# Kernel tuning notes

Hardware: AMD Instinct MI355X
Metric: run time of the kernel (lower is better)

Reference implementation:

```python
import jax, jax.numpy as jnp
import numpy as np
import math

D_MODEL = 1024
NUM_HEADS = 16
HEAD_DIM = D_MODEL // NUM_HEADS
BATCH = 2
SEQ = 2048
THETA = 10000.0


def _rope_tables(seq_len, head_dim, theta=THETA):
    inv_freq = 1.0 / theta ** (jnp.arange(0, head_dim, 2, dtype=jnp.float32) / head_dim)
    pos = jnp.arange(seq_len, dtype=jnp.float32)
    freqs = jnp.outer(pos, inv_freq)                 # [S, hd/2]
    emb = jnp.concatenate([freqs, freqs], axis=-1)   # [S, hd]
    return jnp.cos(emb), jnp.sin(emb)


def _rotate_half(x):
    x1, x2 = jnp.split(x, 2, axis=-1)
    return jnp.concatenate([-x2, x1], axis=-1)


def setup_inputs() -> dict:
    key = jax.random.key(0)
    k1, k2, k3 = jax.random.split(key, 3)
    x = jax.random.normal(k1, (BATCH, SEQ, D_MODEL), dtype=jnp.float32)
    # causal mask: 1 where attend allowed, 0 where masked
    mask = jnp.tril(jnp.ones((SEQ, SEQ), dtype=jnp.int32))[None, None]
    w_qkv = jax.random.normal(k2, (D_MODEL, 3 * D_MODEL), dtype=jnp.float32) / math.sqrt(D_MODEL)
    w_out = jax.random.normal(k3, (D_MODEL, D_MODEL), dtype=jnp.float32) / math.sqrt(D_MODEL)
    return {"x": x, "mask": mask, "w_qkv": w_qkv, "w_out": w_out}


def reference(x, mask, w_qkv, w_out):
    B, S, _ = x.shape
    qkv = x @ w_qkv                                          # [B,S,3*D]
    qkv = qkv.reshape(B, S, 3, NUM_HEADS, HEAD_DIM)
    qkv = jnp.transpose(qkv, (2, 0, 3, 1, 4))                # [3,B,H,S,hd]
    q, k, v = qkv[0], qkv[1], qkv[2]
    cos, sin = _rope_tables(S, HEAD_DIM)                     # [S,hd]
    cos = cos[None, None]; sin = sin[None, None]
    q = q * cos + _rotate_half(q) * sin
    k = k * cos + _rotate_half(k) * sin
    scores = jnp.einsum('bhqd,bhkd->bhqk', q, k) / math.sqrt(HEAD_DIM)
    scores = jnp.where(mask == 0, -jnp.inf, scores)
    attn = jax.nn.softmax(scores, axis=-1)                   # dropout p=0 (eval)
    out = jnp.einsum('bhqk,bhkd->bhqd', attn, v)             # [B,H,S,hd]
    out = jnp.transpose(out, (0, 2, 1, 3)).reshape(B, S, D_MODEL)
    return out @ w_out
```

## Files before the change

### kernel.cpp

```cpp
#include <hip/hip_runtime.h>

typedef __bf16 bf16;
typedef __bf16 bf16x4 __attribute__((ext_vector_type(4)));
typedef __bf16 bf16x8 __attribute__((ext_vector_type(8)));
typedef short s16x4 __attribute__((ext_vector_type(4)));
typedef float f32x4 __attribute__((ext_vector_type(4)));

constexpr int BATCH = 2;
constexpr int SEQ   = 2048;
constexpr int DMODEL= 1024;
constexpr int NH    = 16;
constexpr int HD    = 64;
constexpr int M_ROWS= BATCH * SEQ;
constexpr int N_QKV = 3 * DMODEL;

#if defined(__HIP_DEVICE_COMPILE__) && __has_builtin(__builtin_amdgcn_exp2f)
#define EXP2(x) __builtin_amdgcn_exp2f(x)
#else
#define EXP2(x) exp2f(x)
#endif

__device__ __forceinline__ void gl_lds16(const bf16* g, bf16* l) {
  __builtin_amdgcn_global_load_lds(
      (const __attribute__((address_space(1))) unsigned int*)g,
      (__attribute__((address_space(3))) unsigned int*)l, 16, 0, 0);
}

__device__ __forceinline__ f32x4 mfma_16x16x16_bf16(bf16x4 a, bf16x4 b,
                                                    f32x4 c) {
#if defined(__HIP_DEVICE_COMPILE__)
  union { bf16x4 h; s16x4 s; } ua{a}, ub{b};
  return __builtin_amdgcn_mfma_f32_16x16x16bf16_1k(ua.s, ub.s, c, 0, 0, 0);
#else
  return c;
#endif
}

__global__ __launch_bounds__(256) void prep_kernel(
    const float* __restrict__ x, const float* __restrict__ w_qkv,
    const float* __restrict__ w_out, bf16* __restrict__ xb,
    bf16* __restrict__ WqkvT, bf16* __restrict__ WoutT) {
  const int bx = blockIdx.x, t = threadIdx.x;
  if (bx < 2048) {
    const int i = (bx * 256 + t) * 8;
    float4 f0 = *(const float4*)&x[i];
    float4 f1 = *(const float4*)&x[i + 4];
    bf16x8 v;
    v[0] = (bf16)f0.x; v[1] = (bf16)f0.y; v[2] = (bf16)f0.z; v[3] = (bf16)f0.w;
    v[4] = (bf16)f1.x; v[5] = (bf16)f1.y; v[6] = (bf16)f1.z; v[7] = (bf16)f1.w;
    *(bf16x8*)&xb[i] = v;
    return;
  }
  __shared__ float tile[32][33];
  const float* src;
  bf16* dst;
  int R, C, c0, r0;
  if (bx < 5120) {
    const int idx = bx - 2048;
    src = w_qkv; dst = WqkvT; R = DMODEL; C = N_QKV;
    c0 = (idx % 96) * 32; r0 = (idx / 96) * 32;
  } else {
    const int idx = bx - 5120;
    src = w_out; dst = WoutT; R = DMODEL; C = DMODEL;
    c0 = (idx & 31) * 32; r0 = (idx >> 5) * 32;
  }
  const int r = t >> 3, c4 = (t & 7) * 4;
  {
    float4 f = *(const float4*)&src[(size_t)(r0 + r) * C + c0 + c4];
    tile[r][c4 + 0] = f.x; tile[r][c4 + 1] = f.y;
    tile[r][c4 + 2] = f.z; tile[r][c4 + 3] = f.w;
  }
  __syncthreads();
  {
    bf16x4 v;
#pragma unroll
    for (int j = 0; j < 4; j++) v[j] = (bf16)tile[c4 + j][r];
    *(bf16x4*)&dst[(size_t)(c0 + r) * R + r0 + c4] = v;
  }
}

__global__ __launch_bounds__(256) void gemm_out64(
    const bf16* __restrict__ A, const bf16* __restrict__ BT,
    float* __restrict__ C, int M, int N, int K) {
  __shared__ bf16 As[2][2048];
  __shared__ bf16 Bs[2][4096];
  const int t = threadIdx.x;
  const int m0 = blockIdx.y * 64;
  const int n0 = blockIdx.x * 128;
  const int w = t >> 6, lane = t & 63, g = lane >> 4, li = lane & 15;
  const int r0w = (w & 1) * 32, c0w = (w >> 1) * 64;
  f32x4 acc[2][4] = {};
  const int ia = w * 64 + lane;
  const int ra = ia >> 2, ca = (ia & 3) * 8;
  const int ib0 = (w * 2 + 0) * 64 + lane, ib1 = (w * 2 + 1) * 64 + lane;
  const int rb0 = ib0 >> 2, cb0 = (ib0 & 3) * 8;
  const int rb1 = ib1 >> 2, cb1 = (ib1 & 3) * 8;

#define OUT_STAGE(buf, k0)                                                   \
  {                                                                          \
    gl_lds16(&A[(size_t)(m0 + ra) * K + (k0) + ca], &As[buf][w * 512]);      \
    gl_lds16(&BT[(size_t)(n0 + rb0) * K + (k0) + cb0],                       \
             &Bs[buf][(w * 2 + 0) * 512]);                                   \
    gl_lds16(&BT[(size_t)(n0 + rb1) * K + (k0) + cb1],                       \
             &Bs[buf][(w * 2 + 1) * 512]);                                   \
  }

  OUT_STAGE(0, 0);
  __syncthreads();
  for (int it = 0; it < 32; ++it) {
    const int cur = it & 1;
    if (it < 31) OUT_STAGE(cur ^ 1, (it + 1) * 32);
    bf16x8 a[2], b[4];
#pragma unroll
    for (int mt = 0; mt < 2; mt++)
      a[mt] = *(const bf16x8*)&As[cur][(r0w + mt * 16 + li) * 32 + g * 8];
#pragma unroll
    for (int nt = 0; nt < 4; nt++)
      b[nt] = *(const bf16x8*)&Bs[cur][(c0w + nt * 16 + li) * 32 + g * 8];
#pragma unroll
    for (int mt = 0; mt < 2; mt++)
#pragma unroll
      for (int nt = 0; nt < 4; nt++)
        acc[mt][nt] = __builtin_amdgcn_mfma_f32_16x16x32_bf16(
            a[mt], b[nt], acc[mt][nt], 0, 0, 0);
    __syncthreads();
  }
#undef OUT_STAGE

#pragma unroll
  for (int mt = 0; mt < 2; mt++)
#pragma unroll
    for (int nt = 0; nt < 4; nt++)
#pragma unroll
      for (int r = 0; r < 4; r++) {
        const int m = m0 + r0w + mt * 16 + g * 4 + r;
        const int n = n0 + c0w + nt * 16 + li;
        C[(size_t)m * N + n] = acc[mt][nt][r];
      }
}

__global__ __launch_bounds__(256) void gemm_qkv_rope(
    const bf16* __restrict__ A, const bf16* __restrict__ BT,
    bf16* __restrict__ Qb, bf16* __restrict__ Kb, bf16* __restrict__ Vt) {
  constexpr int K = DMODEL;
  __shared__ bf16 smem[16384];
  const int t = threadIdx.x;
  const int m0 = blockIdx.y * 128;
  const int n0 = blockIdx.x * 128;
  const int w = t >> 6, lane = t & 63, g = lane >> 4, li = lane & 15;
  const int r0w = (w & 1) * 64, c0w = (w >> 1) * 64;
  f32x4 acc[4][4] = {};

  const int i0 = (w * 2 + 0) * 64 + lane, i1 = (w * 2 + 1) * 64 + lane;
  const int sr0 = i0 >> 2, sc0 = (i0 & 3) * 8;
  const int sr1 = i1 >> 2, sc1 = (i1 & 3) * 8;

#define QKV_STAGE(buf, k0)                                                   \
  {                                                                          \
    bf16* Asb = smem + (buf)*4096;                                           \
    bf16* Bsb = smem + 8192 + (buf)*4096;                                    \
    gl_lds16(&A[(size_t)(m0 + sr0) * K + (k0) + sc0],                        \
             &Asb[(w * 2 + 0) * 512]);                                       \
    gl_lds16(&A[(size_t)(m0 + sr1) * K + (k0) + sc1],                        \
             &Asb[(w * 2 + 1) * 512]);                                       \
    gl_lds16(&BT[(size_t)(n0 + sr0) * K + (k0) + sc0],                       \
             &Bsb[(w * 2 + 0) * 512]);                                       \
    gl_lds16(&BT[(size_t)(n0 + sr1) * K + (k0) + sc1],                       \
             &Bsb[(w * 2 + 1) * 512]);                                       \
  }

  QKV_STAGE(0, 0);
  __syncthreads();
  for (int it = 0; it < 32; ++it) {
    const int cur = it & 1;
    if (it < 31) QKV_STAGE(cur ^ 1, (it + 1) * 32);
    const bf16* Asb = smem + cur * 4096;
    const bf16* Bsb = smem + 8192 + cur * 4096;
    bf16x8 a[4], b[4];
#pragma unroll
    for (int mt = 0; mt < 4; mt++)
      a[mt] = *(const bf16x8*)&Asb[(r0w + mt * 16 + li) * 32 + g * 8];
#pragma unroll
    for (int nt = 0; nt < 4; nt++)
      b[nt] = *(const bf16x8*)&Bsb[(c0w + nt * 16 + li) * 32 + g * 8];
#pragma unroll
    for (int mt = 0; mt < 4; mt++)
#pragma unroll
      for (int nt = 0; nt < 4; nt++)
        acc[mt][nt] = __builtin_amdgcn_mfma_f32_16x16x32_bf16(
            a[mt], b[nt], acc[mt][nt], 0, 0, 0);
    __syncthreads();
  }
#undef QKV_STAGE

  const int region = n0 >> 10;
  const int b = m0 >> 11;
  const int h = ((n0 + c0w) >> 6) & 15;
  const size_t bh = (size_t)(b * NH + h);

  if (region < 2) {
    bf16* dst = region == 0 ? Qb : Kb;
    const float outsc = region == 0 ? 0.125f * 1.44269504f : 1.f;
    const float L = 13.287712379549449f;
    const float if0 = exp2f(-(float)(2 * li) / 64.f * L);
    const float if1 = exp2f(-(float)(2 * (li + 16)) / 64.f * L);
    bf16* lw = smem + w * 2112;
#pragma unroll
    for (int pass = 0; pass < 2; pass++) {
      __syncthreads();
#pragma unroll
      for (int mtl = 0; mtl < 2; mtl++) {
        const int mt = pass * 2 + mtl;
#pragma unroll
        for (int r = 0; r < 4; r++) {
          const int s = (m0 + r0w + mt * 16 + g * 4 + r) & (SEQ - 1);
          float cs[2], sn[2];
          __sincosf((float)s * if0, &sn[0], &cs[0]);
          __sincosf((float)s * if1, &sn[1], &cs[1]);
#pragma unroll
          for (int nt = 0; nt < 4; nt++) {
            const int par = nt & 1;
            const float a = acc[mt][nt][r];
            const float ap = acc[mt][nt ^ 2][r];
            const float v = (nt < 2) ? a * cs[par] - ap * sn[par]
                                     : a * cs[par] + ap * sn[par];
            lw[(mtl * 16 + g * 4 + r) * 66 + nt * 16 + li] =
                (bf16)(v * outsc);
          }
        }
      }
      __syncthreads();
      const int rowl = lane >> 1, dh = (lane & 1) * 32;
      const int s = (m0 + r0w + pass * 32 + rowl) & (SEQ - 1);
      bf16* gdst = &dst[(bh * SEQ + s) * HD + dh];
      const bf16* lsrc = &lw[rowl * 66 + dh];
#pragma unroll
      for (int c = 0; c < 4; c++)
        *(bf16x8*)&gdst[c * 8] = *(const bf16x8*)&lsrc[c * 8];
    }
  } else {
#pragma unroll
    for (int mt = 0; mt < 4; mt++)
#pragma unroll
      for (int nt = 0; nt < 4; nt++) {
        const int s = (m0 + r0w + mt * 16 + g * 4) & (SEQ - 1);
        const int d = nt * 16 + li;
        bf16x4 v;
#pragma unroll
        for (int r = 0; r < 4; r++) v[r] = (bf16)acc[mt][nt][r];
        *(bf16x4*)&Vt[(bh * HD + d) * SEQ + s] = v;
      }
  }
}

__device__ const unsigned char CHUNK_TAB[80] = {
    124, 125, 126, 127,
    120, 121, 122, 116, 117, 118, 112, 113, 114, 108, 109, 110,
    104, 105, 106, 100, 101, 102, 96,  97,  98,  92,  93,  94,
    88,  89,  84,  85,  80,  81,  76,  77,  72,  73,  68,  69,
    64,  65,  60,  61,
    56,  52,  48,  44,  40,  36,  32,  28,
    24,  57,  90,  123, 20,  53,  86,  119, 16,  49,  82,  115,
    12,  45,  78,  111, 8,   41,  74,  107, 4,   37,  70,  103,
    0,   33,  66,  99};

__global__ __launch_bounds__(256, 5) void flash_attn15(
    const bf16* __restrict__ Q, const bf16* __restrict__ Kb,
    const bf16* __restrict__ Vt, bf16* __restrict__ Oout,
    float* __restrict__ Opart, float* __restrict__ Lpart) {
  const int bx = blockIdx.x;
  const unsigned char e = CHUNK_TAB[bx >> 5];
  const int qt = e >> 2, kch = e & 3;
  const int bh = bx & 31;
  const int q0 = qt * 64;
  const int jlo = kch * 8;
  const int jhi = min(jlo + 8, qt + 1);
  const int t = threadIdx.x, w = t >> 6, lane = t & 63, g = lane >> 4,
            li = lane & 15;

  __shared__ bf16 Ks[2][4096];
  __shared__ bf16 Vs[2][4096];

  const bf16* Qh = Q  + (size_t)bh * SEQ * HD;
  const bf16* Kh = Kb + (size_t)bh * SEQ * HD;
  const bf16* Vh = Vt + (size_t)bh * HD * SEQ;

  const int qw = q0 + w * 16;

  bf16x8 qf[2];
#pragma unroll
  for (int ks = 0; ks < 2; ks++)
    qf[ks] = *(const bf16x8*)&Qh[(size_t)(qw + li) * HD + ks * 32 + g * 8];

  f32x4 o[4] = {};
  f32x4 o4  = {};
  bf16x4 ones;
#pragma unroll
  for (int r = 0; r < 4; r++) ones[r] = (bf16)1.f;

  int koffB[2][4];
#pragma unroll
  for (int ks = 0; ks < 2; ks++)
#pragma unroll
    for (int nt = 0; nt < 4; nt++) {
      const int rK = nt * 16 + li;
      const int pK = rK * 8 + ((ks * 4 + g) ^ (li & 7));
      koffB[ks][nt] = pK * 16;
    }
  int voffB[4][4];
#pragma unroll
  for (int nt = 0; nt < 4; nt++)
#pragma unroll
    for (int dt = 0; dt < 4; dt++) {
      const int rV = dt * 16 + li;
      const int cg = nt * 2 + (g >> 1);
      const int pV = rV * 8 + (cg ^ (rV & 7));
      voffB[nt][dt] = pV * 16 + (g & 1) * 8;
    }

  const int p0 = w * 128 + lane, p1 = p0 + 64;
  const int sr0 = p0 >> 3, sc0 = ((p0 & 7) ^ (sr0 & 7)) * 8;
  const int sr1 = p1 >> 3, sc1 = ((p1 & 7) ^ (sr1 & 7)) * 8;
  const int lo0 = w * 1024, lo1 = w * 1024 + 512;

  {
    const int jn = jlo * 64;
    gl_lds16(&Kh[(size_t)(jn + sr0) * HD + sc0], &Ks[jlo & 1][lo0]);
    gl_lds16(&Kh[(size_t)(jn + sr1) * HD + sc1], &Ks[jlo & 1][lo1]);
    gl_lds16(&Vh[(size_t)sr0 * SEQ + jn + sc0], &Vs[jlo & 1][lo0]);
    gl_lds16(&Vh[(size_t)sr1 * SEQ + jn + sc1], &Vs[jlo & 1][lo1]);
  }
  __syncthreads();

  for (int ti = jlo; ti < jhi; ++ti) {
    const int cur = ti & 1, nxt = cur ^ 1;
    const char* ksb = (const char*)&Ks[cur][0];
    const char* vsb = (const char*)&Vs[cur][0];
    if (ti + 1 < jhi) {
      const int jn = ti * 64 + 64;
      gl_lds16(&Kh[(size_t)(jn + sr0) * HD + sc0], &Ks[nxt][lo0]);
      gl_lds16(&Kh[(size_t)(jn + sr1) * HD + sc1], &Ks[nxt][lo1]);
      gl_lds16(&Vh[(size_t)sr0 * SEQ + jn + sc0], &Vs[nxt][lo0]);
      gl_lds16(&Vh[(size_t)sr1 * SEQ + jn + sc1], &Vs[nxt][lo1]);
    }

    if (ti < qt) {
      f32x4 sacc[4] = {};
      __builtin_amdgcn_s_setprio(1);
#pragma unroll
      for (int ks = 0; ks < 2; ks++)
#pragma unroll
        for (int nt = 0; nt < 4; nt++) {
          bf16x8 kf = *(const bf16x8*)(ksb + koffB[ks][nt]);
          sacc[nt] = __builtin_amdgcn_mfma_f32_16x16x32_bf16(kf, qf[ks],
                                                             sacc[nt], 0, 0, 0);
        }
      __builtin_amdgcn_s_setprio(0);

      bf16x4 pf[4];
#pragma unroll
      for (int nt = 0; nt < 4; nt++)
#pragma unroll
        for (int r = 0; r < 4; r++) pf[nt][r] = (bf16)EXP2(sacc[nt][r]);

      __builtin_amdgcn_s_setprio(1);
#pragma unroll
      for (int nt = 0; nt < 4; nt++) {
        o4 = mfma_16x16x16_bf16(ones, pf[nt], o4);
#pragma unroll
        for (int dt = 0; dt < 4; dt++) {
          bf16x4 vfrag = *(const bf16x4*)(vsb + voffB[nt][dt]);
          o[dt] = mfma_16x16x16_bf16(vfrag, pf[nt], o[dt]);
        }
      }
      __builtin_amdgcn_s_setprio(0);
    } else {
      f32x4 sacc[4] = {};
      __builtin_amdgcn_s_setprio(1);
#pragma unroll
      for (int ks = 0; ks < 2; ks++)
#pragma unroll
        for (int nt = 0; nt < 4; nt++) {
          if (nt > w) continue;
          bf16x8 kf = *(const bf16x8*)(ksb + koffB[ks][nt]);
          sacc[nt] = __builtin_amdgcn_mfma_f32_16x16x32_bf16(kf, qf[ks],
                                                             sacc[nt], 0, 0, 0);
        }
      __builtin_amdgcn_s_setprio(0);

      bf16x4 pf[4];
#pragma unroll
      for (int nt = 0; nt < 4; nt++) {
        if (nt > w) continue;
#pragma unroll
        for (int r = 0; r < 4; r++) {
          float v = sacc[nt][r];
          if (nt == w) {
            const int kk = nt * 16 + g * 4 + r;
            v = (kk <= w * 16 + li) ? v : -1e30f;
          }
          pf[nt][r] = (bf16)EXP2(v);
        }
      }

      __builtin_amdgcn_s_setprio(1);
#pragma unroll
      for (int nt = 0; nt < 4; nt++) {
        if (nt > w) continue;
        o4 = mfma_16x16x16_bf16(ones, pf[nt], o4);
#pragma unroll
        for (int dt = 0; dt < 4; dt++) {
          bf16x4 vfrag = *(const bf16x4*)(vsb + voffB[nt][dt]);
          o[dt] = mfma_16x16x16_bf16(vfrag, pf[nt], o[dt]);
        }
      }
      __builtin_amdgcn_s_setprio(0);
    }
    __syncthreads();
  }

  if (qt <= 7) {
    const float inv_l = 1.f / o4[0];
    const int b = bh >> 4, h = bh & 15;
    const int s = qw + li;
#pragma unroll
    for (int dt = 0; dt < 4; dt++) {
      bf16x4 ov;
#pragma unroll
      for (int r = 0; r < 4; r++) ov[r] = (bf16)(o[dt][r] * inv_l);
      *(bf16x4*)&Oout[((size_t)(b * SEQ + s)) * DMODEL + h * 64 + dt * 16 +
                      g * 4] = ov;
    }
  } else {
    const int s = qw + li;
    int off;
    if (qt < 16)       off = (s - 512) * 2 + kch;
    else if (qt < 24)  off = 1024 + (s - 1024) * 3 + kch;
    else               off = 2560 + (s - 1536) * 4 + kch;
    const size_t slot = (size_t)bh * 4608 + off;
    if (g == 0) Lpart[slot] = o4[0];
    float* od = &Opart[slot * 64];
#pragma unroll
    for (int dt = 0; dt < 4; dt++)
      *(f32x4*)&od[dt * 16 + g * 4] = o[dt];
  }
}

__global__ __launch_bounds__(256) void attn_merge2(
    const float* __restrict__ Opart, const float* __restrict__ Lpart,
    bf16* __restrict__ attn) {
  const int gi = blockIdx.x * 256 + threadIdx.x;
  const int row = gi >> 3;
  const int d0 = (gi & 7) * 8;
  const int bh = row / 1536, srel = row - bh * 1536;
  const int b = bh >> 4, h = bh & 15, s = srel + 512;
  int off0, nc;
  if (srel < 512)       { off0 = srel * 2;                nc = 2; }
  else if (srel < 1024) { off0 = 1024 + (srel - 512) * 3; nc = 3; }
  else                  { off0 = 2560 + (srel - 1024) * 4; nc = 4; }
  const size_t base = (size_t)bh * 4608 + off0;
  float lsum = 0.f;
  float acc[8] = {};
  for (int c = 0; c < nc; c++) {
    lsum += Lpart[base + c];
    const float* p = &Opart[(base + c) * 64 + d0];
    float4 a0 = *(const float4*)p;
    float4 a1 = *(const float4*)(p + 4);
    acc[0] += a0.x; acc[1] += a0.y; acc[2] += a0.z; acc[3] += a0.w;
    acc[4] += a1.x; acc[5] += a1.y; acc[6] += a1.z; acc[7] += a1.w;
  }
  const float inv = 1.f / lsum;
  bf16x8 v;
#pragma unroll
  for (int i = 0; i < 8; i++) v[i] = (bf16)(acc[i] * inv);
  *(bf16x8*)&attn[((size_t)(b * SEQ + s)) * DMODEL + h * 64 + d0] = v;
}

extern "C" void kernel_launch(void* const* d_in, const int* in_sizes, int n_in,
                              void* d_out, int out_size, void* d_ws,
                              size_t ws_size, hipStream_t stream) {
  const float* x     = (const float*)d_in[0];
  const float* w_qkv = (const float*)d_in[2];
  const float* w_out = (const float*)d_in[3];
  float* out = (float*)d_out;

  char* ws = (char*)d_ws;
  bf16* WqkvT = (bf16*)(ws);
  bf16* WoutT = (bf16*)(ws + 6291456);
  bf16* xb    = (bf16*)(ws + 8388608);
  bf16* Qb    = (bf16*)(ws + 16777216);
  bf16* Kbuf  = (bf16*)(ws + 25165824);
  bf16* Vt    = (bf16*)(ws + 33554432);
  bf16* attn  = (bf16*)(ws + 41943040);
  float* Opart= (float*)(ws + 50331648);
  float* Lpart= (float*)(ws + 88080384);

  prep_kernel<<<dim3(6144), 256, 0, stream>>>(x, w_qkv, w_out, xb, WqkvT,
                                              WoutT);
  gemm_qkv_rope<<<dim3(N_QKV / 128, M_ROWS / 128), 256, 0, stream>>>(
      xb, WqkvT, Qb, Kbuf, Vt);
  flash_attn15<<<dim3(2560), 256, 0, stream>>>(Qb, Kbuf, Vt, attn, Opart,
                                               Lpart);
  attn_merge2<<<dim3(1536), 256, 0, stream>>>(Opart, Lpart, attn);
  gemm_out64<<<dim3(DMODEL / 128, M_ROWS / 64), 256, 0, stream>>>(
      attn, WoutT, out, M_ROWS, DMODEL, DMODEL);
}
```

Before: 194.2 us.

## Triple-buffer QKV GEMM with vmcnt waits; single-buffer output GEMM

The QKV+RoPE GEMM moves from a double-buffered to a three-stage LDS pipeline. It prefetches two K-slices ahead and replaces __syncthreads with explicit s_waitcnt vmcnt(4) plus s_barrier, so one slice of global-to-LDS loads can stay in flight across the barrier. This should hide more load latency, at the cost of 48KB of LDS per block, which may lower occupancy. Separately, the output-projection GEMM drops its double buffering and becomes a simple load, sync, compute loop, which removes its load/compute overlap.

Result: faster. 190.0 us (-2.2%).

```diff
diff --git a/kernel.cpp b/kernel.cpp
--- a/kernel.cpp
+++ b/kernel.cpp
@@ -82,51 +82,42 @@
 __global__ __launch_bounds__(256) void gemm_out64(
     const bf16* __restrict__ A, const bf16* __restrict__ BT,
     float* __restrict__ C, int M, int N, int K) {
-  __shared__ bf16 As[2][2048];
-  __shared__ bf16 Bs[2][4096];
+  __shared__ bf16 As[64 * 32];
+  __shared__ bf16 Bs[128 * 32];
   const int t = threadIdx.x;
   const int m0 = blockIdx.y * 64;
   const int n0 = blockIdx.x * 128;
   const int w = t >> 6, lane = t & 63, g = lane >> 4, li = lane & 15;
   const int r0w = (w & 1) * 32, c0w = (w >> 1) * 64;
   f32x4 acc[2][4] = {};
-  const int ia = w * 64 + lane;
-  const int ra = ia >> 2, ca = (ia & 3) * 8;
-  const int ib0 = (w * 2 + 0) * 64 + lane, ib1 = (w * 2 + 1) * 64 + lane;
-  const int rb0 = ib0 >> 2, cb0 = (ib0 & 3) * 8;
-  const int rb1 = ib1 >> 2, cb1 = (ib1 & 3) * 8;
-
-#define OUT_STAGE(buf, k0)                                                   \
-  {                                                                          \
-    gl_lds16(&A[(size_t)(m0 + ra) * K + (k0) + ca], &As[buf][w * 512]);      \
-    gl_lds16(&BT[(size_t)(n0 + rb0) * K + (k0) + cb0],                       \
-             &Bs[buf][(w * 2 + 0) * 512]);                                   \
-    gl_lds16(&BT[(size_t)(n0 + rb1) * K + (k0) + cb1],                       \
-             &Bs[buf][(w * 2 + 1) * 512]);                                   \
-  }
-
-  OUT_STAGE(0, 0);
-  __syncthreads();
-  for (int it = 0; it < 32; ++it) {
-    const int cur = it & 1;
-    if (it < 31) OUT_STAGE(cur ^ 1, (it + 1) * 32);
+  for (int k0 = 0; k0 < K; k0 += 32) {
+    __syncthreads();
+    {
+      const int idx = w * 64 + lane;
+      const int row = idx >> 2, col = (idx & 3) * 8;
+      gl_lds16(&A[(size_t)(m0 + row) * K + k0 + col], &As[w * 512]);
+    }
+#pragma unroll
+    for (int c = 0; c < 2; c++) {
+      const int idx = (w * 2 + c) * 64 + lane;
+      const int row = idx >> 2, col = (idx & 3) * 8;
+      gl_lds16(&BT[(size_t)(n0 + row) * K + k0 + col], &Bs[(w * 2 + c) * 512]);
+    }
+    __syncthreads();
     bf16x8 a[2], b[4];
 #pragma unroll
     for (int mt = 0; mt < 2; mt++)
-      a[mt] = *(const bf16x8*)&As[cur][(r0w + mt * 16 + li) * 32 + g * 8];
+      a[mt] = *(const bf16x8*)&As[(r0w + mt * 16 + li) * 32 + g * 8];
 #pragma unroll
     for (int nt = 0; nt < 4; nt++)
-      b[nt] = *(const bf16x8*)&Bs[cur][(c0w + nt * 16 + li) * 32 + g * 8];
+      b[nt] = *(const bf16x8*)&Bs[(c0w + nt * 16 + li) * 32 + g * 8];
 #pragma unroll
     for (int mt = 0; mt < 2; mt++)
 #pragma unroll
       for (int nt = 0; nt < 4; nt++)
         acc[mt][nt] = __builtin_amdgcn_mfma_f32_16x16x32_bf16(
             a[mt], b[nt], acc[mt][nt], 0, 0, 0);
-    __syncthreads();
-  }
-#undef OUT_STAGE
-
+  }
 #pragma unroll
   for (int mt = 0; mt < 2; mt++)
 #pragma unroll
@@ -143,7 +134,7 @@
     const bf16* __restrict__ A, const bf16* __restrict__ BT,
     bf16* __restrict__ Qb, bf16* __restrict__ Kb, bf16* __restrict__ Vt) {
   constexpr int K = DMODEL;
-  __shared__ bf16 smem[16384];
+  __shared__ bf16 smem[24576];
   const int t = threadIdx.x;
   const int m0 = blockIdx.y * 128;
   const int n0 = blockIdx.x * 128;
@@ -157,8 +148,8 @@
 
 #define QKV_STAGE(buf, k0)                                                   \
   {                                                                          \
-    bf16* Asb = smem + (buf)*4096;                                           \
-    bf16* Bsb = smem + 8192 + (buf)*4096;                                    \
+    bf16* Asb = smem + (buf) * 4096;                                         \
+    bf16* Bsb = smem + 12288 + (buf) * 4096;                                 \
     gl_lds16(&A[(size_t)(m0 + sr0) * K + (k0) + sc0],                        \
              &Asb[(w * 2 + 0) * 512]);                                       \
     gl_lds16(&A[(size_t)(m0 + sr1) * K + (k0) + sc1],                        \
@@ -170,12 +161,15 @@
   }
 
   QKV_STAGE(0, 0);
-  __syncthreads();
+  QKV_STAGE(1, 32);
+  asm volatile("s_waitcnt vmcnt(4)" ::: "memory");
+  asm volatile("s_barrier" ::: "memory");
+
+  int cur = 0;
   for (int it = 0; it < 32; ++it) {
-    const int cur = it & 1;
-    if (it < 31) QKV_STAGE(cur ^ 1, (it + 1) * 32);
+    if (it + 2 < 32) QKV_STAGE((it + 2) % 3, (it + 2) * 32);
     const bf16* Asb = smem + cur * 4096;
-    const bf16* Bsb = smem + 8192 + cur * 4096;
+    const bf16* Bsb = smem + 12288 + cur * 4096;
     bf16x8 a[4], b[4];
 #pragma unroll
     for (int mt = 0; mt < 4; mt++)
@@ -189,7 +183,12 @@
       for (int nt = 0; nt < 4; nt++)
         acc[mt][nt] = __builtin_amdgcn_mfma_f32_16x16x32_bf16(
             a[mt], b[nt], acc[mt][nt], 0, 0, 0);
-    __syncthreads();
+    if (it + 2 < 32)
+      asm volatile("s_waitcnt vmcnt(4)" ::: "memory");
+    else
+      asm volatile("s_waitcnt vmcnt(0)" ::: "memory");
+    asm volatile("s_barrier" ::: "memory");
+    cur = (cur == 2) ? 0 : cur + 1;
   }
 #undef QKV_STAGE
 
```
